# Performance work log

Measured on AMD Instinct MI355X. Metric: run time of the kernel, lower is better.

## Reference

```python
import jax, jax.numpy as jnp
import numpy as np


def setup_inputs() -> dict:
    key = jax.random.key(0)
    kx, kb, kc, ka, kd = jax.random.split(key, 5)
    B, L, D, N = 8, 4096, 1024, 128
    x = jax.random.normal(kx, (B, L, D), jnp.float32)
    B_w = jax.random.normal(kb, (N, D), jnp.float32) * 0.01  # nn.Linear(d_model->d_state).weight
    C_w = jax.random.normal(kc, (D, N), jnp.float32)         # nn.Linear(d_state->d_model).weight
    # stable negative log_A (HiPPO init gives -|diag|+0.1 < 0)
    log_A = -jax.random.uniform(ka, (N,), jnp.float32) * 3.0 - 0.1
    D_param = jax.random.normal(kd, (D,), jnp.float32)
    return dict(x=x, B_w=B_w, C_w=C_w, log_A=log_A, D_param=D_param)


def reference(x, B_w, C_w, log_A, D_param):
    # x: (B,L,D); B_w: (N,D); C_w: (D,N); log_A: (N,); D_param: (D,)
    A = jnp.exp(log_A)                                   # (N,) diagonal transition
    x_proj = jnp.einsum('bld,nd->bln', x, B_w)           # B @ x  -> (B,L,N)

    def step(h, u):                                      # h_t = A*h_{t-1} + u_t
        h = A * h + u
        return h, h

    h0 = jnp.zeros((x.shape[0], B_w.shape[0]), x.dtype)  # (B,N)
    _, hs = jax.lax.scan(step, h0, jnp.swapaxes(x_proj, 0, 1))  # hs: (L,B,N)

    y = jnp.einsum('lbn,dn->bld', hs, C_w)               # C @ h -> (B,L,D)
    y = y + x * D_param                                  # skip term D*x

    last = x_proj[:, -1, :]                              # (B,N)
    final_state = jnp.broadcast_to(last.mean(axis=0, keepdims=True), last.shape)
    return y, final_state
```

## Files before the change

kernel.cpp:

```cpp
#include <hip/hip_runtime.h>


typedef _Float16 half8 __attribute__((ext_vector_type(8)));
typedef _Float16 half4 __attribute__((ext_vector_type(4)));
typedef float f32x4 __attribute__((ext_vector_type(4)));

#define BDIM 8
#define LDIM 4096
#define DDIM 1024
#define NDIM 128
#define MTOT (BDIM * LDIM)
#define CHUNK 128
#define NCHUNK (LDIM / CHUNK)
#define TOTCHUNK (BDIM * NCHUNK)

__device__ __forceinline__ void dma16(const void* g, void* l) {
    __builtin_amdgcn_global_load_lds((const __attribute__((address_space(1))) void*)g,
                                     (__attribute__((address_space(3))) void*)l, 16, 0, 0);
}

__global__ __launch_bounds__(256) void prep(const float* __restrict__ x,
                                            const float* __restrict__ Bw,
                                            const float* __restrict__ Cw,
                                            _Float16* __restrict__ Bwh,
                                            _Float16* __restrict__ Cwh,
                                            float* __restrict__ out) {
    const int blk = blockIdx.x;
    const int t = threadIdx.x;
    if (blk < 128) {
        const int n = blk;
        float s = 0.f;
        const float* br = Bw + n * DDIM;
        for (int b = 0; b < BDIM; ++b) {
            const float* xr = x + ((size_t)b * LDIM + (LDIM - 1)) * DDIM;
            for (int k = t; k < DDIM; k += 256)
                s = fmaf(xr[k], br[k], s);
        }
        __shared__ float red[256];
        red[t] = s;
        __syncthreads();
        for (int off = 128; off > 0; off >>= 1) {
            if (t < off) red[t] += red[t + off];
            __syncthreads();
        }
        if (t == 0) {
            float v = red[0] * 0.125f;
            for (int b = 0; b < BDIM; ++b)
                out[(size_t)MTOT * DDIM + b * NDIM + n] = v;
        }
    } else {
        const int base = (blk - 128) * 4096;
#pragma unroll
        for (int j = 0; j < 4; ++j) {
            int e = base + j * 1024 + t * 4;
            const float* src;
            _Float16* dst;
            if (e < 131072) { src = Bw + e; dst = Bwh + e; }
            else            { src = Cw + (e - 131072); dst = Cwh + (e - 131072); }
            float4 v = *reinterpret_cast<const float4*>(src);
            half4 h = { (_Float16)v.x, (_Float16)v.y, (_Float16)v.z, (_Float16)v.w };
            *reinterpret_cast<half4*>(dst) = h;
        }
    }
}

__global__ __launch_bounds__(256) void gemm1(const float* __restrict__ x,
                                             const _Float16* __restrict__ Bwh,
                                             float* __restrict__ xp) {
    __shared__ _Float16 As[64 * 32];
    __shared__ _Float16 Bs[128 * 32];
    const int t = threadIdx.x;
    const int row0 = blockIdx.x * 64;
    const int wave = t >> 6, lane = t & 63;
    const int wr = (wave >> 1) * 32, wc = (wave & 1) * 64;
    const int lrow = lane & 15, kq = (lane >> 4) * 8;

    f32x4 acc[2][4] = {};

    for (int kk = 0; kk < DDIM; kk += 32) {
#pragma unroll
        for (int j = 0; j < 2; ++j) {
            int i = t + 256 * j;
            int r = i >> 3, c4 = i & 7;
            float4 v = *reinterpret_cast<const float4*>(&x[(row0 + r) * DDIM + kk + c4 * 4]);
            half4 h = { (_Float16)v.x, (_Float16)v.y, (_Float16)v.z, (_Float16)v.w };
            *reinterpret_cast<half4*>(&As[r * 32 + c4 * 4]) = h;
        }
#pragma unroll
        for (int inst = 0; inst < 2; ++inst) {
            int s = inst * 256 + t;
            int r = s >> 2, c8 = s & 3;
            dma16(&Bwh[r * DDIM + kk + c8 * 8], &Bs[(inst * 256 + wave * 64) * 8]);
        }
        __syncthreads();

        half8 bf[4];
#pragma unroll
        for (int ct = 0; ct < 4; ++ct)
            bf[ct] = *reinterpret_cast<const half8*>(&Bs[(wc + ct * 16 + lrow) * 32 + kq]);
#pragma unroll
        for (int rt = 0; rt < 2; ++rt) {
            half8 af = *reinterpret_cast<const half8*>(&As[(wr + rt * 16 + lrow) * 32 + kq]);
#pragma unroll
            for (int ct = 0; ct < 4; ++ct)
                acc[rt][ct] = __builtin_amdgcn_mfma_f32_16x16x32_f16(af, bf[ct], acc[rt][ct], 0, 0, 0);
        }
        __syncthreads();
    }

    const int q4 = (lane >> 4) * 4;
#pragma unroll
    for (int rt = 0; rt < 2; ++rt)
#pragma unroll
        for (int ct = 0; ct < 4; ++ct) {
            int col = wc + ct * 16 + lrow;
#pragma unroll
            for (int i = 0; i < 4; ++i)
                xp[(row0 + wr + rt * 16 + q4 + i) * NDIM + col] = acc[rt][ct][i];
        }
}

__global__ void scan_agg(const float* __restrict__ xp, const float* __restrict__ logA,
                         float* __restrict__ agg) {
    const int chunk = blockIdx.x;
    const int n = threadIdx.x;
    const float A = expf(logA[n]);
    const float* u = xp + chunk * CHUNK * NDIM + n;
    float h = 0.f;
#pragma unroll 4
    for (int j = 0; j < CHUNK; ++j)
        h = fmaf(A, h, u[j * NDIM]);
    agg[chunk * NDIM + n] = h;
}

__global__ void scan_carry(const float* __restrict__ agg, const float* __restrict__ logA,
                           float* __restrict__ hprev) {
    const int idx = blockIdx.x * blockDim.x + threadIdx.x;
    const int b = idx >> 7, n = idx & 127;
    const float A128 = expf(128.f * logA[n]);
    float c = 0.f;
    for (int ch = 0; ch < NCHUNK; ++ch) {
        int g = (b * NCHUNK + ch) * NDIM + n;
        hprev[g] = c;
        c = fmaf(A128, c, agg[g]);
    }
}

__global__ void scan_final(const float* __restrict__ xp, const float* __restrict__ logA,
                           const float* __restrict__ hprev, _Float16* __restrict__ hs) {
    const int chunk = blockIdx.x;
    const int n = threadIdx.x;
    const float A = expf(logA[n]);
    float h = hprev[chunk * NDIM + n];
    const float* u = xp + chunk * CHUNK * NDIM + n;
    _Float16* o = hs + chunk * CHUNK * NDIM + n;
#pragma unroll 4
    for (int j = 0; j < CHUNK; ++j) {
        h = fmaf(A, h, u[j * NDIM]);
        o[j * NDIM] = (_Float16)h;
    }
}

#define BUFW 132
__global__ __launch_bounds__(256) void gemm2(const _Float16* __restrict__ hs,
                                             const _Float16* __restrict__ Cwh,
                                             const float* __restrict__ x,
                                             const float* __restrict__ Dp,
                                             float* __restrict__ y) {
    __shared__ char smem[65536];
    __shared__ __align__(16) float DpS[128];
    _Float16* hsP = (_Float16*)smem;
    _Float16* CsP = (_Float16*)(smem + 32768);

    const int t = threadIdx.x;
    const int row0 = blockIdx.x * 128;
    const int col0 = blockIdx.y * 128;
    const int wave = t >> 6, lane = t & 63;
    const int wr = (wave >> 1) * 64, wc = (wave & 1) * 64;
    const int lrow = lane & 15, kq = (lane >> 4) * 8;

    if (t < 128) DpS[t] = Dp[col0 + t];

#pragma unroll
    for (int inst = 0; inst < 8; ++inst) {
        int s = inst * 256 + t;
        int kb = s >> 9, r = (s & 511) >> 2, c8 = s & 3;
        void* ldst = &hsP[(inst * 256 + wave * 64) * 8];
        dma16(&hs[(row0 + r) * NDIM + kb * 32 + c8 * 8], ldst);
    }
#pragma unroll
    for (int inst = 0; inst < 8; ++inst) {
        int s = inst * 256 + t;
        int kb = s >> 9, r = (s & 511) >> 2, c8 = s & 3;
        void* ldst = &CsP[(inst * 256 + wave * 64) * 8];
        dma16(&Cwh[(col0 + r) * NDIM + kb * 32 + c8 * 8], ldst);
    }
    __syncthreads();

    f32x4 acc[4][4] = {};
#pragma unroll
    for (int kb = 0; kb < 4; ++kb) {
        half8 bf[4];
#pragma unroll
        for (int ct = 0; ct < 4; ++ct)
            bf[ct] = *reinterpret_cast<const half8*>(&CsP[kb * 4096 + (wc + ct * 16 + lrow) * 32 + kq]);
#pragma unroll
        for (int rt = 0; rt < 4; ++rt) {
            half8 af = *reinterpret_cast<const half8*>(&hsP[kb * 4096 + (wr + rt * 16 + lrow) * 32 + kq]);
#pragma unroll
            for (int ct = 0; ct < 4; ++ct)
                acc[rt][ct] = __builtin_amdgcn_mfma_f32_16x16x32_f16(af, bf[ct], acc[rt][ct], 0, 0, 0);
        }
    }

    float* buf = (float*)smem;
    const int q4 = (lane >> 4) * 4;
#pragma unroll
    for (int half_ = 0; half_ < 2; ++half_) {
        __syncthreads();
        if ((wr >> 6) == half_) {
#pragma unroll
            for (int rt = 0; rt < 4; ++rt)
#pragma unroll
                for (int ct = 0; ct < 4; ++ct) {
                    int col = wc + ct * 16 + lrow;
#pragma unroll
                    for (int i = 0; i < 4; ++i)
                        buf[(rt * 16 + q4 + i) * BUFW + col] = acc[rt][ct][i];
                }
        }
        __syncthreads();
#pragma unroll
        for (int j = 0; j < 8; ++j) {
            int idx = t + 256 * j;
            int row = idx >> 5, c4 = idx & 31;
            int grow = row0 + half_ * 64 + row;
            float4 a = *reinterpret_cast<const float4*>(&buf[row * BUFW + c4 * 4]);
            float4 xv = *reinterpret_cast<const float4*>(&x[(size_t)grow * DDIM + col0 + c4 * 4]);
            float4 dp = *reinterpret_cast<const float4*>(&DpS[c4 * 4]);
            float4 o;
            o.x = a.x + xv.x * dp.x;
            o.y = a.y + xv.y * dp.y;
            o.z = a.z + xv.z * dp.z;
            o.w = a.w + xv.w * dp.w;
            *reinterpret_cast<float4*>(&y[(size_t)grow * DDIM + col0 + c4 * 4]) = o;
        }
    }
}

extern "C" void kernel_launch(void* const* d_in, const int* in_sizes, int n_in,
                              void* d_out, int out_size, void* d_ws, size_t ws_size,
                              hipStream_t stream) {
    const float* x    = (const float*)d_in[0];
    const float* Bw   = (const float*)d_in[1];
    const float* Cw   = (const float*)d_in[2];
    const float* logA = (const float*)d_in[3];
    const float* Dp   = (const float*)d_in[4];
    float* out = (float*)d_out;

    char* ws = (char*)d_ws;
    float*    xp    = (float*)   (ws);
    _Float16* hs    = (_Float16*)(ws + 16777216);
    float*    agg   = (float*)   (ws + 25165824);
    float*    hprev = (float*)   (ws + 25296896);
    _Float16* Bwh   = (_Float16*)(ws + 25427968);
    _Float16* Cwh   = (_Float16*)(ws + 25690112);

    prep<<<192, 256, 0, stream>>>(x, Bw, Cw, Bwh, Cwh, out);
    gemm1<<<MTOT / 64, 256, 0, stream>>>(x, Bwh, xp);
    scan_agg<<<TOTCHUNK, 128, 0, stream>>>(xp, logA, agg);
    scan_carry<<<4, 256, 0, stream>>>(agg, logA, hprev);
    scan_final<<<TOTCHUNK, 128, 0, stream>>>(xp, logA, hprev, hs);
    gemm2<<<dim3(MTOT / 128, DDIM / 128), 256, 0, stream>>>(hs, Cwh, x, Dp, out);
}
```

Before: 329.7 us.

## Load GEMM operands directly from global memory, halve scan chunk size

Both GEMM kernels stop staging operands in LDS with async DMA and syncthreads. Each lane now loads its MFMA fragments straight from global memory (x converted to fp16 in registers in gemm1), and gemm2 keeps LDS only for the epilogue and reads D_param into registers. The scan chunk size drops from 128 to 64, which doubles parallelism for the scan kernels and lengthens the carry loop, and the scan loops are unrolled more deeply. The workspace offsets are moved to fit the larger agg buffer. Removing LDS staging cuts barriers and LDS traffic, but adds redundant, less coalesced global loads that now depend on cache reuse.

After: 345.6 us. 4.8% more time.

```diff
diff --git a/kernel.cpp b/kernel.cpp
--- a/kernel.cpp
+++ b/kernel.cpp
@@ -10,14 +10,9 @@
 #define DDIM 1024
 #define NDIM 128
 #define MTOT (BDIM * LDIM)
-#define CHUNK 128
+#define CHUNK 64
 #define NCHUNK (LDIM / CHUNK)
 #define TOTCHUNK (BDIM * NCHUNK)
-
-__device__ __forceinline__ void dma16(const void* g, void* l) {
-    __builtin_amdgcn_global_load_lds((const __attribute__((address_space(1))) void*)g,
-                                     (__attribute__((address_space(3))) void*)l, 16, 0, 0);
-}
 
 __global__ __launch_bounds__(256) void prep(const float* __restrict__ x,
                                             const float* __restrict__ Bw,
@@ -67,45 +62,39 @@
 __global__ __launch_bounds__(256) void gemm1(const float* __restrict__ x,
                                              const _Float16* __restrict__ Bwh,
                                              float* __restrict__ xp) {
-    __shared__ _Float16 As[64 * 32];
-    __shared__ _Float16 Bs[128 * 32];
     const int t = threadIdx.x;
     const int row0 = blockIdx.x * 64;
     const int wave = t >> 6, lane = t & 63;
     const int wr = (wave >> 1) * 32, wc = (wave & 1) * 64;
     const int lrow = lane & 15, kq = (lane >> 4) * 8;
 
+    const float* xA0 = x + (size_t)(row0 + wr + lrow) * DDIM + kq;
+    const float* xA1 = xA0 + (size_t)16 * DDIM;
+    const _Float16* Bb = Bwh + (size_t)(wc + lrow) * DDIM + kq;
+
     f32x4 acc[2][4] = {};
 
+#pragma unroll 4
     for (int kk = 0; kk < DDIM; kk += 32) {
-#pragma unroll
-        for (int j = 0; j < 2; ++j) {
-            int i = t + 256 * j;
-            int r = i >> 3, c4 = i & 7;
-            float4 v = *reinterpret_cast<const float4*>(&x[(row0 + r) * DDIM + kk + c4 * 4]);
-            half4 h = { (_Float16)v.x, (_Float16)v.y, (_Float16)v.z, (_Float16)v.w };
-            *reinterpret_cast<half4*>(&As[r * 32 + c4 * 4]) = h;
-        }
-#pragma unroll
-        for (int inst = 0; inst < 2; ++inst) {
-            int s = inst * 256 + t;
-            int r = s >> 2, c8 = s & 3;
-            dma16(&Bwh[r * DDIM + kk + c8 * 8], &Bs[(inst * 256 + wave * 64) * 8]);
-        }
-        __syncthreads();
-
-        half8 bf[4];
-#pragma unroll
-        for (int ct = 0; ct < 4; ++ct)
-            bf[ct] = *reinterpret_cast<const half8*>(&Bs[(wc + ct * 16 + lrow) * 32 + kq]);
+        half8 af[2];
 #pragma unroll
         for (int rt = 0; rt < 2; ++rt) {
-            half8 af = *reinterpret_cast<const half8*>(&As[(wr + rt * 16 + lrow) * 32 + kq]);
-#pragma unroll
-            for (int ct = 0; ct < 4; ++ct)
-                acc[rt][ct] = __builtin_amdgcn_mfma_f32_16x16x32_f16(af, bf[ct], acc[rt][ct], 0, 0, 0);
-        }
-        __syncthreads();
+            const float* p = (rt ? xA1 : xA0) + kk;
+            float4 v0 = *reinterpret_cast<const float4*>(p);
+            float4 v1 = *reinterpret_cast<const float4*>(p + 4);
+            half8 h;
+            h[0] = (_Float16)v0.x; h[1] = (_Float16)v0.y;
+            h[2] = (_Float16)v0.z; h[3] = (_Float16)v0.w;
+            h[4] = (_Float16)v1.x; h[5] = (_Float16)v1.y;
+            h[6] = (_Float16)v1.z; h[7] = (_Float16)v1.w;
+            af[rt] = h;
+        }
+#pragma unroll
+        for (int ct = 0; ct < 4; ++ct) {
+            half8 bf = *reinterpret_cast<const half8*>(Bb + (size_t)ct * 16 * DDIM + kk);
+            acc[0][ct] = __builtin_amdgcn_mfma_f32_16x16x32_f16(af[0], bf, acc[0][ct], 0, 0, 0);
+            acc[1][ct] = __builtin_amdgcn_mfma_f32_16x16x32_f16(af[1], bf, acc[1][ct], 0, 0, 0);
+        }
     }
 
     const int q4 = (lane >> 4) * 4;
@@ -127,7 +116,7 @@
     const float A = expf(logA[n]);
     const float* u = xp + chunk * CHUNK * NDIM + n;
     float h = 0.f;
-#pragma unroll 4
+#pragma unroll 16
     for (int j = 0; j < CHUNK; ++j)
         h = fmaf(A, h, u[j * NDIM]);
     agg[chunk * NDIM + n] = h;
@@ -137,12 +126,13 @@
                            float* __restrict__ hprev) {
     const int idx = blockIdx.x * blockDim.x + threadIdx.x;
     const int b = idx >> 7, n = idx & 127;
-    const float A128 = expf(128.f * logA[n]);
+    const float Ac = expf((float)CHUNK * logA[n]);
     float c = 0.f;
+#pragma unroll 8
     for (int ch = 0; ch < NCHUNK; ++ch) {
         int g = (b * NCHUNK + ch) * NDIM + n;
         hprev[g] = c;
-        c = fmaf(A128, c, agg[g]);
+        c = fmaf(Ac, c, agg[g]);
     }
 }
 
@@ -154,7 +144,7 @@
     float h = hprev[chunk * NDIM + n];
     const float* u = xp + chunk * CHUNK * NDIM + n;
     _Float16* o = hs + chunk * CHUNK * NDIM + n;
-#pragma unroll 4
+#pragma unroll 16
     for (int j = 0; j < CHUNK; ++j) {
         h = fmaf(A, h, u[j * NDIM]);
         o[j * NDIM] = (_Float16)h;
@@ -167,11 +157,7 @@
                                              const float* __restrict__ x,
                                              const float* __restrict__ Dp,
                                              float* __restrict__ y) {
-    __shared__ char smem[65536];
-    __shared__ __align__(16) float DpS[128];
-    _Float16* hsP = (_Float16*)smem;
-    _Float16* CsP = (_Float16*)(smem + 32768);
-
+    __shared__ float buf[64 * BUFW];
     const int t = threadIdx.x;
     const int row0 = blockIdx.x * 128;
     const int col0 = blockIdx.y * 128;
@@ -179,41 +165,28 @@
     const int wr = (wave >> 1) * 64, wc = (wave & 1) * 64;
     const int lrow = lane & 15, kq = (lane >> 4) * 8;
 
-    if (t < 128) DpS[t] = Dp[col0 + t];
-
-#pragma unroll
-    for (int inst = 0; inst < 8; ++inst) {
-        int s = inst * 256 + t;
-        int kb = s >> 9, r = (s & 511) >> 2, c8 = s & 3;
-        void* ldst = &hsP[(inst * 256 + wave * 64) * 8];
-        dma16(&hs[(row0 + r) * NDIM + kb * 32 + c8 * 8], ldst);
-    }
-#pragma unroll
-    for (int inst = 0; inst < 8; ++inst) {
-        int s = inst * 256 + t;
-        int kb = s >> 9, r = (s & 511) >> 2, c8 = s & 3;
-        void* ldst = &CsP[(inst * 256 + wave * 64) * 8];
-        dma16(&Cwh[(col0 + r) * NDIM + kb * 32 + c8 * 8], ldst);
-    }
-    __syncthreads();
+    const _Float16* Ab = hs + (size_t)(row0 + wr + lrow) * NDIM + kq;
+    const _Float16* Bb = Cwh + (size_t)(col0 + wc + lrow) * NDIM + kq;
 
     f32x4 acc[4][4] = {};
 #pragma unroll
     for (int kb = 0; kb < 4; ++kb) {
-        half8 bf[4];
+        half8 af[4], bf[4];
+#pragma unroll
+        for (int rt = 0; rt < 4; ++rt)
+            af[rt] = *reinterpret_cast<const half8*>(Ab + (size_t)rt * 16 * NDIM + kb * 32);
 #pragma unroll
         for (int ct = 0; ct < 4; ++ct)
-            bf[ct] = *reinterpret_cast<const half8*>(&CsP[kb * 4096 + (wc + ct * 16 + lrow) * 32 + kq]);
-#pragma unroll
-        for (int rt = 0; rt < 4; ++rt) {
-            half8 af = *reinterpret_cast<const half8*>(&hsP[kb * 4096 + (wr + rt * 16 + lrow) * 32 + kq]);
+            bf[ct] = *reinterpret_cast<const half8*>(Bb + (size_t)ct * 16 * NDIM + kb * 32);
+#pragma unroll
+        for (int rt = 0; rt < 4; ++rt)
 #pragma unroll
             for (int ct = 0; ct < 4; ++ct)
-                acc[rt][ct] = __builtin_amdgcn_mfma_f32_16x16x32_f16(af, bf[ct], acc[rt][ct], 0, 0, 0);
-        }
-    }
-
-    float* buf = (float*)smem;
+                acc[rt][ct] = __builtin_amdgcn_mfma_f32_16x16x32_f16(af[rt], bf[ct], acc[rt][ct], 0, 0, 0);
+    }
+
+    float4 dp = *reinterpret_cast<const float4*>(&Dp[col0 + (t & 31) * 4]);
+
     const int q4 = (lane >> 4) * 4;
 #pragma unroll
     for (int half_ = 0; half_ < 2; ++half_) {
@@ -237,7 +210,6 @@
             int grow = row0 + half_ * 64 + row;
             float4 a = *reinterpret_cast<const float4*>(&buf[row * BUFW + c4 * 4]);
             float4 xv = *reinterpret_cast<const float4*>(&x[(size_t)grow * DDIM + col0 + c4 * 4]);
-            float4 dp = *reinterpret_cast<const float4*>(&DpS[c4 * 4]);
             float4 o;
             o.x = a.x + xv.x * dp.x;
             o.y = a.y + xv.y * dp.y;
@@ -262,9 +234,9 @@
     float*    xp    = (float*)   (ws);
     _Float16* hs    = (_Float16*)(ws + 16777216);
     float*    agg   = (float*)   (ws + 25165824);
-    float*    hprev = (float*)   (ws + 25296896);
-    _Float16* Bwh   = (_Float16*)(ws + 25427968);
-    _Float16* Cwh   = (_Float16*)(ws + 25690112);
+    float*    hprev = (float*)   (ws + 25427968);
+    _Float16* Bwh   = (_Float16*)(ws + 25690112);
+    _Float16* Cwh   = (_Float16*)(ws + 25952256);
 
     prep<<<192, 256, 0, stream>>>(x, Bw, Cw, Bwh, Cwh, out);
     gemm1<<<MTOT / 64, 256, 0, stream>>>(x, Bwh, xp);
```
